# Performance work log

Measured on AMD Instinct MI355X. Metric: run time of the kernel, lower is better.

## Reference

```python
import jax, jax.numpy as jnp
import numpy as np

K = 7        # upsample_kernel_size
S = 2        # upscale_factor
EK = K - 2   # encoder kernel size (5)


def conv2d(x, w, b, padding):
    out = jax.lax.conv_general_dilated(
        x, w, window_strides=(1, 1), padding=[(padding, padding), (padding, padding)],
        dimension_numbers=('NCHW', 'OIHW', 'NCHW'))
    return out + b[None, :, None, None]


def pixel_shuffle(x, s):
    B, C, H, W = x.shape
    oc = C // (s * s)
    x = x.reshape(B, oc, s, s, H, W)
    x = x.transpose(0, 1, 4, 2, 5, 3)
    return x.reshape(B, oc, H * s, W * s)


def carafe(x, kmap, k, s):
    # x: [B,C,H,W], kmap: [B,k*k,H*s,W*s] softmax-normalized
    B, C, H, W = x.shape
    pad = k // 2
    xp = jnp.pad(x, ((0, 0), (0, 0), (pad, pad), (pad, pad)))
    # k^2 shifted views -> [B,C,k2,H,W]
    patches = jnp.stack([xp[:, :, dy:dy + H, dx:dx + W]
                         for dy in range(k) for dx in range(k)], axis=2)
    # output pixel (i,j) reads source (i//s, j//s): factor kmap spatial dims
    km = kmap.reshape(B, k * k, H, s, W, s)
    out = jnp.einsum('bcnhw,bnhpwq->bchpwq', patches, km)
    return out.reshape(B, C, H * s, W * s)


def setup_inputs() -> dict:
    key = jax.random.key(0)
    k1, k2, k3 = jax.random.split(key, 3)
    B, C, H, W = 4, 256, 64, 64
    comp_c = 64
    enc_out = (S * K) ** 2  # 196
    x = jax.random.normal(k1, (B, C, H, W), dtype=jnp.float32)
    w_comp = jax.random.normal(k2, (comp_c, C, 1, 1), dtype=jnp.float32) * (1.0 / np.sqrt(C))
    b_comp = jnp.zeros((comp_c,), dtype=jnp.float32)
    w_enc = jax.random.normal(k3, (enc_out, comp_c, EK, EK), dtype=jnp.float32) * (1.0 / np.sqrt(comp_c * EK * EK))
    b_enc = jnp.zeros((enc_out,), dtype=jnp.float32)
    return {'x': x, 'w_comp': w_comp, 'b_comp': b_comp, 'w_enc': w_enc, 'b_enc': b_enc}


def reference(x, w_comp, b_comp, w_enc, b_enc):
    compressed = conv2d(x, w_comp, b_comp, padding=0)
    content = conv2d(compressed, w_enc, b_enc, padding=EK // 2)
    upsampled = pixel_shuffle(content, S)            # [B, k^2, H*s, W*s]
    kernel_map = jax.nn.softmax(upsampled, axis=1)
    return carafe(x, kernel_map, K, S)
```

## Files before the change

kernel.cpp:

```cpp
#include <hip/hip_runtime.h>
#include <math.h>
#include <stdint.h>

#define B_   4
#define C_   256
#define H_   64
#define W_   64
#define CC_  64
#define OE_  196
#define OH_  128
#define OW_  128
#define XH_  72
#define NWB_ 10

typedef uint32_t u32;
typedef unsigned short u16;
typedef __attribute__((ext_vector_type(8))) short bf16x8;
typedef __attribute__((ext_vector_type(4))) float f32x4;
typedef __attribute__((ext_vector_type(4))) u32 u32x4;
typedef __attribute__((ext_vector_type(2))) u32 u32x2;

__device__ __forceinline__ u16 f2bf(float f) {
  u32 u = __builtin_bit_cast(u32, f);
  u32 r = (u + 0x7FFFu + ((u >> 16) & 1u)) >> 16;
  return (u16)r;
}

__global__ __launch_bounds__(256) void prep_weights(
    const float* __restrict__ w_comp, const float* __restrict__ w_enc,
    u16* __restrict__ wfrag, u16* __restrict__ wcf,
    u16* __restrict__ xw8) {
  int idx = blockIdx.x * 256 + threadIdx.x;
  if (idx < 50 * 14 * 64) {
    int lane = idx & 63;
    int mt   = (idx >> 6) % 14;
    int ks   = idx / (14 * 64);
    int o    = mt * 16 + (lane & 15);
    int tap  = ks >> 1, s = ks & 1;
    int ky   = tap / 5, kx = tap % 5;
    int cb   = s * 32 + (lane >> 4) * 8;
    u32 pk[4];
    #pragma unroll
    for (int p = 0; p < 4; ++p) {
      u16 lo = 0, hi = 0;
      if (o < OE_) {
        lo = f2bf(w_enc[((o * CC_ + cb + 2 * p) * 5 + ky) * 5 + kx]);
        hi = f2bf(w_enc[((o * CC_ + cb + 2 * p + 1) * 5 + ky) * 5 + kx]);
      }
      pk[p] = (u32)lo | ((u32)hi << 16);
    }
    *reinterpret_cast<u32x4*>(wfrag + (size_t)idx * 8) =
        *reinterpret_cast<u32x4*>(pk);
  }
  if (idx < 8 * 4 * 64) {
    int lane = idx & 63;
    int mt   = (idx >> 6) & 3;
    int ks   = idx >> 8;
    int o    = mt * 16 + (lane & 15);
    int cb   = ks * 32 + (lane >> 4) * 8;
    u32 pk[4];
    #pragma unroll
    for (int p = 0; p < 4; ++p) {
      u16 lo = f2bf(w_comp[o * C_ + cb + 2 * p]);
      u16 hi = f2bf(w_comp[o * C_ + cb + 2 * p + 1]);
      pk[p] = (u32)lo | ((u32)hi << 16);
    }
    *reinterpret_cast<u32x4*>(wcf + (size_t)idx * 8) =
        *reinterpret_cast<u32x4*>(pk);
  }
  {
    u32x4 z = {0, 0, 0, 0};
    for (int i = idx; i < B_ * XH_ * NWB_ * C_; i += 65536)
      *reinterpret_cast<u32x4*>(xw8 + (size_t)i * 8) = z;
  }
}

__global__ __launch_bounds__(256) void compress_k(
    const float* __restrict__ x, const u16* __restrict__ wcf,
    const float* __restrict__ b_comp, u16* __restrict__ comp,
    u16* __restrict__ xw8) {
  __shared__ float xs[C_ * 20];
  int t   = threadIdx.x;
  int gid = blockIdx.x;
  int wq  = gid & 3;
  int bh  = gid >> 2;
  int b = bh >> 6, h = bh & 63;
  int w0 = wq * 16;

  const float* xrow = x + (size_t)b * C_ * H_ * W_ + (size_t)h * W_ + w0;
  for (int i = t; i < 1024; i += 256) {
    int c = i >> 2, q = i & 3;
    f32x4 v = *reinterpret_cast<const f32x4*>(xrow + (size_t)c * H_ * W_ + q * 4);
    *reinterpret_cast<f32x4*>(xs + c * 20 + q * 4) = v;
  }
  __syncthreads();

  int wv   = __builtin_amdgcn_readfirstlane(t >> 6);
  int lane = t & 63;
  int w    = lane & 15;
  int lg   = lane >> 4;

  bf16x8 af[8];
  #pragma unroll
  for (int ks = 0; ks < 8; ++ks)
    af[ks] = *reinterpret_cast<const bf16x8*>(
        wcf + (((size_t)ks * 4 + wv) * 64 + lane) * 8);

  f32x4 acc = {0.f, 0.f, 0.f, 0.f};
  #pragma unroll
  for (int ks = 0; ks < 8; ++ks) {
    short vv[8];
    #pragma unroll
    for (int j = 0; j < 8; ++j)
      vv[j] = (short)f2bf(xs[(ks * 32 + lg * 8 + j) * 20 + w]);
    bf16x8 bf = (bf16x8){vv[0], vv[1], vv[2], vv[3], vv[4], vv[5], vv[6], vv[7]};
    acc = __builtin_amdgcn_mfma_f32_16x16x32_bf16(af[ks], bf, acc, 0, 0, 0);
  }

  {
    int cc0 = wv * 16 + lg * 4;
    f32x4 bias = *reinterpret_cast<const f32x4*>(b_comp + cc0);
    u32 p0 = (u32)f2bf(acc[0] + bias[0]) | ((u32)f2bf(acc[1] + bias[1]) << 16);
    u32 p1 = (u32)f2bf(acc[2] + bias[2]) | ((u32)f2bf(acc[3] + bias[3]) << 16);
    u32x2 pk = {p0, p1};
    *reinterpret_cast<u32x2*>(comp + ((size_t)bh * 64 + w0 + w) * CC_ + cc0) = pk;
  }

  {
    int ww = t & 15, cq = t >> 4;
    int wp = w0 + ww + 3;
    size_t base = (((size_t)(b * XH_ + h + 3)) * NWB_ + (wp >> 3)) * (C_ * 8) + (wp & 7);
    #pragma unroll
    for (int i = 0; i < 16; ++i) {
      int c = cq * 16 + i;
      xw8[base + c * 8] = f2bf(xs[c * 20 + ww]);
    }
  }
}

#define ELG_ 32256

__device__ __forceinline__ void enc_lda(
    bf16x8 (&a)[2], const u16* __restrict__ wfrag,
    int ks, int mtbase, int lane) {
  #pragma unroll
  for (int mm = 0; mm < 2; ++mm)
    a[mm] = *reinterpret_cast<const bf16x8*>(
        wfrag + (((size_t)ks * 14 + mtbase + mm) * 64 + lane) * 8);
}

__device__ __forceinline__ void enc_step(
    int ks, const char* lds, const bf16x8 (&a)[2], f32x4 (&acc)[2][2],
    int nlane, int kq) {
  int tap = ks >> 1, s = ks & 1;
  int ky = tap / 5, kx = tap % 5;
  bf16x8 bf[2];
  #pragma unroll
  for (int nt = 0; nt < 2; ++nt) {
    int col = nt * 16 + nlane + kx;
    int byte = (((ky * 36 + col) * 64 + s * 32 + kq * 8) * 2) ^ ((col & 7) << 4);
    bf[nt] = *reinterpret_cast<const bf16x8*>(lds + byte);
  }
  #pragma unroll
  for (int mm = 0; mm < 2; ++mm)
    #pragma unroll
    for (int nt = 0; nt < 2; ++nt)
      acc[mm][nt] = __builtin_amdgcn_mfma_f32_16x16x32_bf16(
          a[mm], bf[nt], acc[mm][nt], 0, 0, 0);
}

__global__ __launch_bounds__(512) void enc_mfma_k(
    const u16* __restrict__ comp, const u16* __restrict__ wfrag,
    const float* __restrict__ b_enc, u16* __restrict__ smax) {
  __shared__ __align__(16) char lds[ELG_];

  int t   = threadIdx.x;
  int bid = blockIdx.x;
  int swz = (bid & 7) * 64 + (bid >> 3);
  int wh  = swz & 1;
  int bh  = swz >> 1;
  int b = bh >> 6, h = bh & 63;
  int w0 = wh * 32;

  {
    const u16* cbse = comp + (size_t)b * H_ * W_ * CC_;
    for (int i = t; i < 1440; i += 512) {
      int q = i & 7, colr = i >> 3;
      int col = colr % 36, r = colr / 36;
      int hh = h - 2 + r, gw = w0 - 2 + col;
      u32x4 v = {0, 0, 0, 0};
      if ((unsigned)hh < H_ && (unsigned)gw < W_)
        v = *reinterpret_cast<const u32x4*>(cbse + ((size_t)hh * W_ + gw) * CC_ + q * 8);
      int byte = ((r * 36 + col) * 128 + q * 16) ^ ((col & 7) << 4);
      *reinterpret_cast<u32x4*>(lds + byte) = v;
    }
  }
  __syncthreads();

  int wv    = __builtin_amdgcn_readfirstlane(t >> 6);
  int lane  = t & 63;
  int nlane = lane & 15, kq = lane >> 4;
  int mtbase = wv * 2;

  f32x4 acc[2][2];
  #pragma unroll
  for (int mm = 0; mm < 2; ++mm)
    #pragma unroll
    for (int nt = 0; nt < 2; ++nt) acc[mm][nt] = (f32x4){0.f, 0.f, 0.f, 0.f};

  if (wv < 7) {
    bf16x8 abuf[4][2];
    #pragma unroll
    for (int p = 0; p < 4; ++p) enc_lda(abuf[p], wfrag, p, mtbase, lane);
    #pragma unroll
    for (int ks = 0; ks < 50; ++ks) {
      enc_step(ks, lds, abuf[ks & 3], acc, nlane, kq);
      if (ks < 46) enc_lda(abuf[ks & 3], wfrag, ks + 4, mtbase, lane);
    }
  }

  __syncthreads();
  float* lg = (float*)lds;
  if (wv < 7) {
    #pragma unroll
    for (int mm = 0; mm < 2; ++mm) {
      #pragma unroll
      for (int nt = 0; nt < 2; ++nt) {
        #pragma unroll
        for (int r = 0; r < 4; ++r) {
          int m  = (mtbase + mm) * 16 + kq * 4 + r;
          int px = nt * 16 + nlane;
          lg[m * 36 + px] = acc[mm][nt][r] + (m < OE_ ? b_enc[m] : 0.f);
        }
      }
    }
  }
  __syncthreads();

  if (t < 128) {
    int px = t & 31, rr = t >> 5;
    float v[49];
    float mx = -1e30f;
    #pragma unroll
    for (int n = 0; n < 49; ++n) {
      v[n] = lg[(4 * n + rr) * 36 + px];
      mx = fmaxf(mx, v[n]);
    }
    float sum = 0.f;
    #pragma unroll
    for (int n = 0; n < 49; ++n) { v[n] = __expf(v[n] - mx); sum += v[n]; }
    float inv = 1.f / sum;
    u16* so = smax + ((size_t)bh * 64 + w0 + px) * OE_;
    #pragma unroll
    for (int n = 0; n < 49; ++n) so[n * 4 + rr] = f2bf(v[n] * inv);
  }
}

__device__ __forceinline__ void carafe_lda(
    bf16x8 (&buf)[4], const u16* __restrict__ xb,
    int c, int h, int wb0, int lg) {
  #pragma unroll
  for (int ks = 0; ks < 4; ++ks) {
    int dy = ks * 2 + (lg >> 1);
    buf[ks] = *reinterpret_cast<const bf16x8*>(
        xb + (((size_t)(h + dy)) * NWB_ + wb0 + (lg & 1)) * (C_ * 8) + c * 8);
  }
}

__global__ __launch_bounds__(256) void carafe_k(
    const u16* __restrict__ xw8, const u16* __restrict__ smax,
    float* __restrict__ out) {
  __shared__ __align__(8) u16 svl[16 * 200];
  int t   = threadIdx.x;
  int bid = blockIdx.x;
  int swz = (bid & 7) * 256 + (bid >> 3);
  int mh  = swz & 1;
  int ws2 = (swz >> 1) & 3;
  int h   = (swz >> 3) & 63;
  int b   = swz >> 9;
  int w00 = ws2 * 16;

  for (int idx = t; idx < 784; idx += 256) {
    int pix = idx / 49, n = idx - pix * 49;
    const u16* sp = smax +
        ((size_t)((b * 64 + h) * 64) + w00 + pix) * OE_ + n * 4;
    *reinterpret_cast<u32x2*>(svl + pix * 200 + n * 4) =
        *reinterpret_cast<const u32x2*>(sp);
  }
  __syncthreads();

  int wv   = t >> 6;
  int lane = t & 63;
  int ws   = wv & 1;
  int mq   = wv >> 1;
  int w0   = w00 + ws * 8;
  int wb0  = w0 >> 3;
  const u16* svb = svl + ws * 8 * 200;

  int col = lane & 15;
  int wi  = col >> 1, q = col & 1;
  int lg  = lane >> 4;
  int mrow = lane & 15;

  bf16x8 bfr[2][4];
  #pragma unroll
  for (int p = 0; p < 2; ++p) {
    #pragma unroll
    for (int ks = 0; ks < 4; ++ks) {
      short v[8];
      #pragma unroll
      for (int j = 0; j < 8; ++j) {
        int k   = ks * 32 + lg * 8 + j;
        int dy  = k >> 4, dxp = k & 15;
        int dx  = dxp - wi;
        u16 s = 0;
        if (dy < 7 && dx >= 0 && dx < 7)
          s = svb[wi * 200 + (dy * 7 + dx) * 4 + 2 * p + q];
        v[j] = (short)s;
      }
      bfr[p][ks] = (bf16x8){v[0], v[1], v[2], v[3], v[4], v[5], v[6], v[7]};
    }
  }

  const u16* xb = xw8 + (size_t)b * XH_ * NWB_ * (C_ * 8);
  int mt0 = mh * 8 + mq * 4;
  bf16x8 bufA[4], bufB[4];
  carafe_lda(bufA, xb, mt0 * 16 + mrow, h, wb0, lg);

  #pragma unroll
  for (int i = 0; i < 4; ++i) {
    int mt = mt0 + i;
    if (i < 3) {
      if (i & 1) carafe_lda(bufA, xb, (mt + 1) * 16 + mrow, h, wb0, lg);
      else       carafe_lda(bufB, xb, (mt + 1) * 16 + mrow, h, wb0, lg);
    }
    f32x4 acc0 = {0.f, 0.f, 0.f, 0.f};
    f32x4 acc1 = {0.f, 0.f, 0.f, 0.f};
    #pragma unroll
    for (int ks = 0; ks < 4; ++ks) {
      bf16x8 af = (i & 1) ? bufB[ks] : bufA[ks];
      acc0 = __builtin_amdgcn_mfma_f32_16x16x32_bf16(af, bfr[0][ks], acc0, 0, 0, 0);
      acc1 = __builtin_amdgcn_mfma_f32_16x16x32_bf16(af, bfr[1][ks], acc1, 0, 0, 0);
    }
    float* o0 = out +
        ((size_t)(b * C_ + mt * 16 + lg * 4) * OH_ + 2 * h) * OW_ + 2 * w0 + col;
    o0[0]                     = acc0[0];
    o0[(size_t)OH_ * OW_]     = acc0[1];
    o0[2 * (size_t)OH_ * OW_] = acc0[2];
    o0[3 * (size_t)OH_ * OW_] = acc0[3];
    float* o1 = o0 + OW_;
    o1[0]                     = acc1[0];
    o1[(size_t)OH_ * OW_]     = acc1[1];
    o1[2 * (size_t)OH_ * OW_] = acc1[2];
    o1[3 * (size_t)OH_ * OW_] = acc1[3];
  }
}

extern "C" void kernel_launch(void* const* d_in, const int* in_sizes, int n_in,
                              void* d_out, int out_size, void* d_ws, size_t ws_size,
                              hipStream_t stream) {
  const float* x      = (const float*)d_in[0];
  const float* w_comp = (const float*)d_in[1];
  const float* b_comp = (const float*)d_in[2];
  const float* w_enc  = (const float*)d_in[3];
  const float* b_enc  = (const float*)d_in[4];
  float* out = (float*)d_out;

  u16* smax  = (u16*)d_ws;
  u16* wfrag = smax + 3211264;
  u16* wcf   = wfrag + 358400;
  u16* comp  = wcf + 16384;
  u16* xw8   = comp + 1048576;

  prep_weights<<<256, 256, 0, stream>>>(w_comp, w_enc, wfrag, wcf, xw8);
  compress_k<<<B_ * H_ * 4, 256, 0, stream>>>(x, wcf, b_comp, comp, xw8);
  enc_mfma_k<<<512, 512, 0, stream>>>(comp, wfrag, b_enc, smax);
  carafe_k<<<2048, 256, 0, stream>>>(xw8, smax, out);
}
```

Baseline: 69.56 us.

## Zero only padding halo of staged input and preload all carafe A tiles

The init kernel now zeroes only the halo rows and columns of the padded bf16 staging buffer rather than the whole buffer, which cuts global write traffic. The interior is presumably overwritten by the compress kernel. The carafe kernel also issues all four A-tile loads up front instead of double-buffering them, so more memory requests are in flight at once. The cost is higher register pressure, which may lower occupancy.

Result: no change. 68.65 us (-1.3%).

```diff
diff --git a/kernel.cpp b/kernel.cpp
--- a/kernel.cpp
+++ b/kernel.cpp
@@ -70,8 +70,21 @@
   }
   {
     u32x4 z = {0, 0, 0, 0};
-    for (int i = idx; i < B_ * XH_ * NWB_ * C_; i += 65536)
-      *reinterpret_cast<u32x4*>(xw8 + (size_t)i * 8) = z;
+    for (int i = idx; i < 1088 * 256; i += 65536) {
+      int zi = i >> 8, ck = i & 255;
+      int b = zi / 272, r = zi % 272;
+      int hp, wb;
+      if (r < 30)      { hp = r / 10;             wb = r % 10; }
+      else if (r < 80) { hp = 67 + (r - 30) / 10; wb = (r - 30) % 10; }
+      else {
+        int rr = r - 80;
+        hp = 3 + rr / 3;
+        int m = rr % 3;
+        wb = (m == 0) ? 0 : (m == 1) ? 8 : 9;
+      }
+      *reinterpret_cast<u32x4*>(
+          xw8 + (((size_t)(b * XH_ + hp)) * NWB_ + wb) * (C_ * 8) + ck * 8) = z;
+    }
   }
 }
 
@@ -324,23 +337,20 @@
 
   const u16* xb = xw8 + (size_t)b * XH_ * NWB_ * (C_ * 8);
   int mt0 = mh * 8 + mq * 4;
-  bf16x8 bufA[4], bufB[4];
-  carafe_lda(bufA, xb, mt0 * 16 + mrow, h, wb0, lg);
+  bf16x8 buf[4][4];
+  #pragma unroll
+  for (int i = 0; i < 4; ++i)
+    carafe_lda(buf[i], xb, (mt0 + i) * 16 + mrow, h, wb0, lg);
 
   #pragma unroll
   for (int i = 0; i < 4; ++i) {
     int mt = mt0 + i;
-    if (i < 3) {
-      if (i & 1) carafe_lda(bufA, xb, (mt + 1) * 16 + mrow, h, wb0, lg);
-      else       carafe_lda(bufB, xb, (mt + 1) * 16 + mrow, h, wb0, lg);
-    }
     f32x4 acc0 = {0.f, 0.f, 0.f, 0.f};
     f32x4 acc1 = {0.f, 0.f, 0.f, 0.f};
     #pragma unroll
     for (int ks = 0; ks < 4; ++ks) {
-      bf16x8 af = (i & 1) ? bufB[ks] : bufA[ks];
-      acc0 = __builtin_amdgcn_mfma_f32_16x16x32_bf16(af, bfr[0][ks], acc0, 0, 0, 0);
-      acc1 = __builtin_amdgcn_mfma_f32_16x16x32_bf16(af, bfr[1][ks], acc1, 0, 0, 0);
+      acc0 = __builtin_amdgcn_mfma_f32_16x16x32_bf16(buf[i][ks], bfr[0][ks], acc0, 0, 0, 0);
+      acc1 = __builtin_amdgcn_mfma_f32_16x16x32_bf16(buf[i][ks], bfr[1][ks], acc1, 0, 0, 0);
     }
     float* o0 = out +
         ((size_t)(b * C_ + mt * 16 + lg * 4) * OH_ + 2 * h) * OW_ + 2 * w0 + col;
```
